# Performance work log

Hardware: AMD Instinct MI355X
Metric: run time of the kernel (lower is better)

## Reference

```python
import jax, jax.numpy as jnp
import numpy as np

# dims
IMG = 24; B = 2; C = 3; N = IMG * IMG + 1        # 577 tokens (patch size 1 + cls)
DIM = 512; DEPTH = 2; H = 8; DH = 64; MLP = 2048; NCLS = 1000
SW = 32      # sliding window size
CB = 16      # compress block size
CS = 4       # compress block sliding stride
SB = 64      # selection block size
KSEL = 4     # num selected blocks


def _ln(x, g, b):
    m = x.mean(-1, keepdims=True)
    v = ((x - m) ** 2).mean(-1, keepdims=True)
    return (x - m) * jax.lax.rsqrt(v + 1e-5) * g + b


# gather rows per (batch, head): t [n, d], i [n, m] -> [n, m, d]
_gather = jax.vmap(jax.vmap(lambda t, i: t[i]))


def _sparse_attn(x, Wq, Wk, Wv, Wg, Wo, kpe, vpe, Wkc, Wvc):
    """Native-sparse-attention (non-causal): compress + top-k block select + sliding window,
    combined with per-head sigmoid gates computed from the input."""
    b, n, _ = x.shape
    split = lambda t: t.reshape(b, n, H, DH).transpose(0, 2, 1, 3)   # [b,h,n,dh]
    q = split(x @ Wq); k = split(x @ Wk); v = split(x @ Wv)
    scale = DH ** -0.5

    # ---- compressed branch: overlapping blocks of size CB, stride CS, MLP-compressed ----
    nc = -(-n // CS)
    pad = (nc - 1) * CS + CB - n
    kp = jnp.pad(k, ((0, 0), (0, 0), (0, pad), (0, 0)))
    vp = jnp.pad(v, ((0, 0), (0, 0), (0, pad), (0, 0)))
    widx = jnp.arange(nc)[:, None] * CS + jnp.arange(CB)[None, :]    # [nc, CB]
    kw = kp[:, :, widx] + kpe                                        # [b,h,nc,CB,dh]
    vw = vp[:, :, widx] + vpe
    ck = kw.reshape(b, H, nc, CB * DH) @ Wkc                         # [b,h,nc,dh]
    cv = vw.reshape(b, H, nc, CB * DH) @ Wvc
    sc = jnp.einsum('bhid,bhjd->bhij', q, ck) * scale                # [b,h,n,nc]
    pc = jax.nn.softmax(sc, axis=-1)
    out_c = jnp.einsum('bhij,bhjd->bhid', pc, cv)

    # ---- selection branch: map compressed-block scores to selection blocks, top-k ----
    ns = -(-n // SB)
    centers = jnp.clip((jnp.arange(nc) * CS + CB // 2) // SB, 0, ns - 1)
    M = jax.nn.one_hot(centers, ns, dtype=pc.dtype)                  # [nc, ns]
    imp = jnp.einsum('bhij,js->bhis', pc, M)                         # [b,h,n,ns]
    _, selb = jax.lax.top_k(imp, KSEL)                               # [b,h,n,KSEL]
    tok = (selb[..., None] * SB + jnp.arange(SB)).reshape(b, H, n, KSEL * SB)
    mask = tok < n
    tokc = jnp.minimum(tok, n - 1)
    kg = _gather(k, tokc)                                            # [b,h,n,KSEL*SB,dh]
    vg = _gather(v, tokc)
    ss = jnp.einsum('bhid,bhikd->bhik', q, kg) * scale
    ss = jnp.where(mask, ss, -jnp.inf)
    ps = jax.nn.softmax(ss, axis=-1)
    out_s = jnp.einsum('bhik,bhikd->bhid', ps, vg)

    # ---- sliding window branch ----
    off = jnp.arange(SW) - SW // 2
    pos = jnp.arange(n)[:, None] + off                               # [n, SW]
    wmask = (pos >= 0) & (pos < n)
    posc = jnp.clip(pos, 0, n - 1)
    kwn = k[:, :, posc]; vwn = v[:, :, posc]                         # [b,h,n,SW,dh]
    sw = jnp.einsum('bhid,bhiwd->bhiw', q, kwn) * scale
    sw = jnp.where(wmask, sw, -jnp.inf)
    pw = jax.nn.softmax(sw, axis=-1)
    out_w = jnp.einsum('bhiw,bhiwd->bhid', pw, vwn)

    # ---- gated combine ----
    g = jax.nn.sigmoid(x @ Wg).reshape(b, n, H, 3).transpose(0, 2, 1, 3)  # [b,h,n,3]
    out = g[..., 0:1] * out_c + g[..., 1:2] * out_s + g[..., 2:3] * out_w
    return out.transpose(0, 2, 1, 3).reshape(b, n, H * DH) @ Wo


def _forward(img, patch_w, patch_b, pos_emb, cls_tok, ln1_g, ln1_b, Wq, Wk, Wv,
             Wg, Wo, kpe, vpe, Wkc, Wvc, ln2_g, ln2_b, ff_w1, ff_b1, ff_w2,
             ff_b2, hln_g, hln_b, head_w, head_b):
    b = img.shape[0]
    # patch size 1: b c h w -> b (h w) c, then linear embed
    x = img.transpose(0, 2, 3, 1).reshape(b, IMG * IMG, C) @ patch_w + patch_b
    x = jnp.concatenate([jnp.broadcast_to(cls_tok, (b, 1, DIM)), x], axis=1)
    x = x + pos_emb[:, :x.shape[1]]
    for l in range(DEPTH):
        h = _ln(x, ln1_g[l], ln1_b[l])
        x = _sparse_attn(h, Wq[l], Wk[l], Wv[l], Wg[l], Wo[l], kpe[l], vpe[l], Wkc[l], Wvc[l]) + x
        h = _ln(x, ln2_g[l], ln2_b[l])
        x = (jax.nn.gelu(h @ ff_w1[l] + ff_b1[l]) @ ff_w2[l] + ff_b2[l]) + x
    x = _ln(x[:, 0], hln_g, hln_b)   # cls pool + head LayerNorm
    return x @ head_w + head_b


def setup_inputs() -> dict:
    key = jax.random.key(0)
    ks = jax.random.split(key, 20)
    rn = lambda k, shape, s=0.02: jax.random.normal(k, shape, dtype=jnp.float32) * s
    d = {}
    d['img'] = jax.random.normal(ks[0], (B, C, IMG, IMG), dtype=jnp.float32)
    d['patch_w'] = rn(ks[1], (C, DIM), 0.2)
    d['patch_b'] = jnp.zeros((DIM,), jnp.float32)
    d['pos_emb'] = rn(ks[2], (1, N, DIM))
    d['cls_tok'] = rn(ks[3], (1, 1, DIM))
    d['ln1_g'] = jnp.ones((DEPTH, DIM), jnp.float32)
    d['ln1_b'] = jnp.zeros((DEPTH, DIM), jnp.float32)
    d['Wq'] = rn(ks[4], (DEPTH, DIM, H * DH))
    d['Wk'] = rn(ks[5], (DEPTH, DIM, H * DH))
    d['Wv'] = rn(ks[6], (DEPTH, DIM, H * DH))
    d['Wg'] = rn(ks[7], (DEPTH, DIM, 3 * H))
    d['Wo'] = rn(ks[8], (DEPTH, H * DH, DIM))
    d['kpe'] = rn(ks[9], (DEPTH, CB, DH))
    d['vpe'] = rn(ks[10], (DEPTH, CB, DH))
    d['Wkc'] = rn(ks[11], (DEPTH, CB * DH, DH))
    d['Wvc'] = rn(ks[12], (DEPTH, CB * DH, DH))
    d['ln2_g'] = jnp.ones((DEPTH, DIM), jnp.float32)
    d['ln2_b'] = jnp.zeros((DEPTH, DIM), jnp.float32)
    d['ff_w1'] = rn(ks[13], (DEPTH, DIM, MLP))
    d['ff_b1'] = jnp.zeros((DEPTH, MLP), jnp.float32)
    d['ff_w2'] = rn(ks[14], (DEPTH, MLP, DIM))
    d['ff_b2'] = jnp.zeros((DEPTH, DIM), jnp.float32)
    d['hln_g'] = jnp.ones((DIM,), jnp.float32)
    d['hln_b'] = jnp.zeros((DIM,), jnp.float32)
    d['head_w'] = rn(ks[15], (DIM, NCLS))
    d['head_b'] = jnp.zeros((NCLS,), jnp.float32)
    return d


def reference(img, patch_w, patch_b, pos_emb, cls_tok, ln1_g, ln1_b, Wq, Wk, Wv,
              Wg, Wo, kpe, vpe, Wkc, Wvc, ln2_g, ln2_b, ff_w1, ff_b1, ff_w2,
              ff_b2, hln_g, hln_b, head_w, head_b):
    return _forward(img, patch_w, patch_b, pos_emb, cls_tok, ln1_g, ln1_b, Wq, Wk, Wv,
                    Wg, Wo, kpe, vpe, Wkc, Wvc, ln2_g, ln2_b, ff_w1, ff_b1, ff_w2,
                    ff_b2, hln_g, hln_b, head_w, head_b)
```

## Files before the change

kernel.cpp:

```cpp
#include <hip/hip_runtime.h>
#include <math.h>


#define NTOK 577
#define DIMD 512
#define NH 8
#define DHD 64
#define NC 145
#define NSB 10
#define KSELD 4
#define SBD 64
#define CBD 16
#define CSD 4
#define SWD 32
#define MLPD 2048
#define NCLSD 1000
#define BATCH 2
#define QKVN 1536
#define QKVNG 1600
#define SFSTRIDE 592
#define SCSTRIDE 160
#define PSTRIDE 832
#define MCKD 2320

typedef unsigned short ushort;
typedef __attribute__((ext_vector_type(8))) short short8;
typedef __attribute__((ext_vector_type(4))) short short4v;
typedef __attribute__((ext_vector_type(4))) float f32x4;

__device__ __forceinline__ ushort bf16_rne(float f) {
  union { float f; unsigned u; } v; v.f = f;
  unsigned u = v.u;
  unsigned r = (u + 0x7fffu + ((u >> 16) & 1u)) >> 16;
  return (ushort)r;
}
__device__ __forceinline__ float bf16_to_f(ushort s) {
  union { unsigned u; float f; } v; v.u = ((unsigned)s) << 16;
  return v.f;
}
__device__ __forceinline__ int imin(int a, int b) { return a < b ? a : b; }
__device__ __forceinline__ int imax(int a, int b) { return a > b ? a : b; }

__global__ void patch_kernel(const float* __restrict__ img, const float* __restrict__ pw,
                             const float* __restrict__ pb, const float* __restrict__ pos,
                             const float* __restrict__ cls, float* __restrict__ x) {
  int idx = blockIdx.x * 256 + threadIdx.x;
  const int total = BATCH * NTOK * DIMD;
  if (idx >= total) return;
  int d = idx & (DIMD - 1);
  int i = (idx / DIMD) % NTOK;
  int b = idx / (DIMD * NTOK);
  float val;
  if (i == 0) {
    val = cls[d];
  } else {
    int p = i - 1;
    val = pb[d];
#pragma unroll
    for (int c = 0; c < 3; ++c)
      val += img[b * 3 * 576 + c * 576 + p] * pw[c * DIMD + d];
  }
  x[idx] = val + pos[i * DIMD + d];
}

__global__ void ln_kernel(const float* __restrict__ x, const float* __restrict__ g,
                          const float* __restrict__ bb, ushort* __restrict__ out_bf) {
  int row = blockIdx.x;
  const float* xr = x + (long)row * DIMD;
  int t = threadIdx.x;
  float a = xr[t], c = xr[t + 256];
  __shared__ float s1[256], s2[256];
  s1[t] = a + c;
  s2[t] = a * a + c * c;
  __syncthreads();
  for (int off = 128; off > 0; off >>= 1) {
    if (t < off) { s1[t] += s1[t + off]; s2[t] += s2[t + off]; }
    __syncthreads();
  }
  float m = s1[0] * (1.0f / 512.0f);
  float var = s2[0] * (1.0f / 512.0f) - m * m;
  float r = rsqrtf(var + 1e-5f);
  out_bf[(long)row * DIMD + t] = bf16_rne((a - m) * r * g[t] + bb[t]);
  out_bf[(long)row * DIMD + t + 256] = bf16_rne((c - m) * r * g[t + 256] + bb[t + 256]);
}

__global__ void wtrans_all_kernel(const float* __restrict__ Wq, const float* __restrict__ Wk,
                                  const float* __restrict__ Wv, const float* __restrict__ Wg,
                                  const float* __restrict__ Wo, const float* __restrict__ Wkc,
                                  const float* __restrict__ Wvc, const float* __restrict__ w1,
                                  const float* __restrict__ w2,
                                  ushort* __restrict__ wqkv_t, ushort* __restrict__ wo_t,
                                  ushort* __restrict__ w1_t, ushort* __restrict__ w2_t,
                                  ushort* __restrict__ wkc_t, ushort* __restrict__ wvc_t) {
  __shared__ float tile[32][33];
  int l = blockIdx.y;
  int t = blockIdx.x;
  const float* W; ushort* Wt; int K, N, bx, by;
  if (t < 768) {
    int which = t >> 8, rr = t & 255;
    W = (which == 0 ? Wq : (which == 1 ? Wk : Wv)) + (long)l * 512 * 512;
    Wt = wqkv_t + (long)l * QKVNG * 512 + which * 512 * 512;
    K = 512; N = 512; bx = rr & 15; by = rr >> 4;
  } else if (t < 1024) {
    int rr = t - 768; W = Wo + (long)l * 512 * 512; Wt = wo_t + (long)l * 512 * 512;
    K = 512; N = 512; bx = rr & 15; by = rr >> 4;
  } else if (t < 2048) {
    int rr = t - 1024; W = w1 + (long)l * 512 * 2048; Wt = w1_t + (long)l * 2048 * 512;
    K = 512; N = 2048; bx = rr & 63; by = rr >> 6;
  } else if (t < 3072) {
    int rr = t - 2048; W = w2 + (long)l * 2048 * 512; Wt = w2_t + (long)l * 512 * 2048;
    K = 2048; N = 512; bx = rr & 15; by = rr >> 4;
  } else if (t < 3104) {
    int rr = t - 3072; W = Wg + (long)l * 512 * 24;
    Wt = wqkv_t + (long)l * QKVNG * 512 + (long)1536 * 512;
    K = 512; N = 24; bx = rr & 1; by = rr >> 1;
  } else if (t < 3168) {
    int rr = t - 3104; W = Wkc + (long)l * 1024 * 64; Wt = wkc_t + (long)l * 64 * 1024;
    K = 1024; N = 64; bx = rr & 1; by = rr >> 1;
  } else {
    int rr = t - 3168; W = Wvc + (long)l * 1024 * 64; Wt = wvc_t + (long)l * 64 * 1024;
    K = 1024; N = 64; bx = rr & 1; by = rr >> 1;
  }
  int k0 = by * 32, n0 = bx * 32;
  int tx = threadIdx.x, ty = threadIdx.y;
#pragma unroll
  for (int r = 0; r < 32; r += 8)
    tile[ty + r][tx] = (n0 + tx < N) ? W[(long)(k0 + ty + r) * N + n0 + tx] : 0.f;
  __syncthreads();
#pragma unroll
  for (int r = 0; r < 32; r += 8)
    Wt[(long)(n0 + ty + r) * K + k0 + tx] = bf16_rne(tile[tx][ty + r]);
}

__global__ __launch_bounds__(256) void mfma_gemm(
    const ushort* __restrict__ A, const ushort* __restrict__ Bt,
    const float* __restrict__ bias,
    float* __restrict__ Cf, ushort* __restrict__ Cbf, float* __restrict__ gb,
    int M, int N, int K, int kSlice, int mode) {
  __shared__ short As[64][72];
  __shared__ short Bs[64][72];
  int tid = threadIdx.x;
  int lane = tid & 63, wave = tid >> 6;
  int wm = wave >> 1, wn = wave & 1;
  int rowBase = blockIdx.y * 64, colBase = blockIdx.x * 64;
  int m = lane & 15, kg = lane >> 4;
  int kBeg = blockIdx.z * kSlice;
  int kEnd = imin(K, kBeg + kSlice);
  f32x4 acc[2][2] = {};
  for (int k0 = kBeg; k0 < kEnd; k0 += 64) {
#pragma unroll
    for (int cc = 0; cc < 2; ++cc) {
      int c = tid * 2 + cc;
      int r = c >> 3, kc = c & 7;
      short8 av = {};
      int gr = rowBase + r;
      if (gr < M) av = *(const short8*)(A + (long)gr * K + k0 + kc * 8);
      *(short8*)&As[r][kc * 8] = av;
      short8 bv = *(const short8*)(Bt + (long)(colBase + r) * K + k0 + kc * 8);
      *(short8*)&Bs[r][kc * 8] = bv;
    }
    __syncthreads();
#pragma unroll
    for (int ks = 0; ks < 2; ++ks) {
      short8 a0 = *(const short8*)&As[wm * 32 + m][ks * 32 + kg * 8];
      short8 a1 = *(const short8*)&As[wm * 32 + 16 + m][ks * 32 + kg * 8];
      short8 b0 = *(const short8*)&Bs[wn * 32 + m][ks * 32 + kg * 8];
      short8 b1 = *(const short8*)&Bs[wn * 32 + 16 + m][ks * 32 + kg * 8];
      acc[0][0] = __builtin_amdgcn_mfma_f32_16x16x32_bf16(a0, b0, acc[0][0], 0, 0, 0);
      acc[0][1] = __builtin_amdgcn_mfma_f32_16x16x32_bf16(a0, b1, acc[0][1], 0, 0, 0);
      acc[1][0] = __builtin_amdgcn_mfma_f32_16x16x32_bf16(a1, b0, acc[1][0], 0, 0, 0);
      acc[1][1] = __builtin_amdgcn_mfma_f32_16x16x32_bf16(a1, b1, acc[1][1], 0, 0, 0);
    }
    __syncthreads();
  }
#pragma unroll
  for (int mt = 0; mt < 2; ++mt)
#pragma unroll
    for (int nt = 0; nt < 2; ++nt) {
      int col = colBase + wn * 32 + nt * 16 + m;
#pragma unroll
      for (int r = 0; r < 4; ++r) {
        int row = rowBase + wm * 32 + mt * 16 + kg * 4 + r;
        if (row >= M) continue;
        float v = acc[mt][nt][r];
        if (mode == 2) {
          if (col < QKVN) Cbf[(long)row * QKVN + col] = bf16_rne(v);
          else if (col < QKVNG) gb[(long)row * 64 + (col - QKVN)] = 1.f / (1.f + __expf(-v));
        } else if (mode == 1) {
          v += bias[col];
          float u = 0.7978845608028654f * (v + 0.044715f * v * v * v);
          v = 0.5f * v * (1.f + tanhf(u));
          Cbf[(long)row * N + col] = bf16_rne(v);
        } else {
          if (bias && blockIdx.z == 0) v += bias[col];
          atomicAdd(&Cf[(long)row * N + col], v);
        }
      }
    }
}

__global__ __launch_bounds__(256) void ckcv_gemm(
    const ushort* __restrict__ kwm, const ushort* __restrict__ vwm,
    const ushort* __restrict__ wkc_t, const ushort* __restrict__ wvc_t,
    ushort* __restrict__ ckb, ushort* __restrict__ Vt) {
  const int K = 1024;
  bool cvpath = blockIdx.z != 0;
  const ushort* A  = cvpath ? wvc_t : kwm;
  const ushort* Bt = cvpath ? vwm : wkc_t;
  int rowBase = cvpath ? 0 : blockIdx.y * 64;
  int colBase = cvpath ? blockIdx.y * 64 : 0;
  int aRows = cvpath ? 64 : MCKD;
  int bRows = cvpath ? MCKD : 64;
  __shared__ short As[64][72];
  __shared__ short Bs[64][72];
  int tid = threadIdx.x;
  int lane = tid & 63, wave = tid >> 6;
  int wm = wave >> 1, wn = wave & 1;
  int m = lane & 15, kg = lane >> 4;
  f32x4 acc[2][2] = {};
  for (int k0 = 0; k0 < K; k0 += 64) {
#pragma unroll
    for (int cc = 0; cc < 2; ++cc) {
      int c = tid * 2 + cc;
      int r = c >> 3, kc = c & 7;
      short8 av = {};
      if (rowBase + r < aRows) av = *(const short8*)(A + (long)(rowBase + r) * K + k0 + kc * 8);
      *(short8*)&As[r][kc * 8] = av;
      short8 bv = {};
      if (colBase + r < bRows) bv = *(const short8*)(Bt + (long)(colBase + r) * K + k0 + kc * 8);
      *(short8*)&Bs[r][kc * 8] = bv;
    }
    __syncthreads();
#pragma unroll
    for (int ks = 0; ks < 2; ++ks) {
      short8 a0 = *(const short8*)&As[wm * 32 + m][ks * 32 + kg * 8];
      short8 a1 = *(const short8*)&As[wm * 32 + 16 + m][ks * 32 + kg * 8];
      short8 b0 = *(const short8*)&Bs[wn * 32 + m][ks * 32 + kg * 8];
      short8 b1 = *(const short8*)&Bs[wn * 32 + 16 + m][ks * 32 + kg * 8];
      acc[0][0] = __builtin_amdgcn_mfma_f32_16x16x32_bf16(a0, b0, acc[0][0], 0, 0, 0);
      acc[0][1] = __builtin_amdgcn_mfma_f32_16x16x32_bf16(a0, b1, acc[0][1], 0, 0, 0);
      acc[1][0] = __builtin_amdgcn_mfma_f32_16x16x32_bf16(a1, b0, acc[1][0], 0, 0, 0);
      acc[1][1] = __builtin_amdgcn_mfma_f32_16x16x32_bf16(a1, b1, acc[1][1], 0, 0, 0);
    }
    __syncthreads();
  }
#pragma unroll
  for (int mt = 0; mt < 2; ++mt)
#pragma unroll
    for (int nt = 0; nt < 2; ++nt) {
      int col = colBase + wn * 32 + nt * 16 + m;
#pragma unroll
      for (int r = 0; r < 4; ++r) {
        int row = rowBase + wm * 32 + mt * 16 + kg * 4 + r;
        float v = acc[mt][nt][r];
        if (!cvpath) {
          if (row < MCKD) ckb[(long)row * DHD + col] = bf16_rne(v);
        } else {
          if (col < MCKD) {
            int z16 = col / NC, j = col - z16 * NC;
            Vt[((long)z16 * 64 + row) * PSTRIDE + 640 + j] = bf16_rne(v);
          }
        }
      }
    }
}

__global__ __launch_bounds__(256) void score_kernel(
    const ushort* __restrict__ qkv_bf, const ushort* __restrict__ ckb,
    ushort* __restrict__ Sf, ushort* __restrict__ Scb, float scale) {
  __shared__ short As[64][72];
  __shared__ short Bs[64][72];
  int z = blockIdx.z;
  int b = z >> 3, h = z & 7;
  int i0 = blockIdx.y * 64;
  int xb = blockIdx.x;
  bool isC = xb >= 10;
  int j0 = (isC ? (xb - 10) : xb) * 64;
  int tid = threadIdx.x;
  int lane = tid & 63, wave = tid >> 6;
  int wm = wave >> 1, wn = wave & 1;
  const ushort* aBase = qkv_bf + (long)b * NTOK * QKVN + h * 64;
  const ushort* bBase = aBase + 512;
  const ushort* cBase = ckb + (long)z * NC * DHD;
#pragma unroll
  for (int rep = 0; rep < 4; ++rep) {
    int row = rep * 16 + (tid >> 4);
    int c4 = tid & 15;
    int gi = i0 + row;
    short4v a16 = {};
    if (gi < NTOK) a16 = *(const short4v*)(aBase + (long)gi * QKVN + c4 * 4);
    *(short4v*)&As[row][c4 * 4] = a16;
    int gj = j0 + row;
    short4v b16 = {};
    if (isC) {
      if (gj < NC) b16 = *(const short4v*)(cBase + (long)gj * DHD + c4 * 4);
    } else {
      if (gj < NTOK) b16 = *(const short4v*)(bBase + (long)gj * QKVN + c4 * 4);
    }
    *(short4v*)&Bs[row][c4 * 4] = b16;
  }
  __syncthreads();
  int m = lane & 15, kg = lane >> 4;
  f32x4 acc[2][2] = {};
#pragma unroll
  for (int ks = 0; ks < 2; ++ks) {
    short8 a0 = *(const short8*)&As[wm * 32 + m][ks * 32 + kg * 8];
    short8 a1 = *(const short8*)&As[wm * 32 + 16 + m][ks * 32 + kg * 8];
    short8 b0 = *(const short8*)&Bs[wn * 32 + m][ks * 32 + kg * 8];
    short8 b1 = *(const short8*)&Bs[wn * 32 + 16 + m][ks * 32 + kg * 8];
    acc[0][0] = __builtin_amdgcn_mfma_f32_16x16x32_bf16(a0, b0, acc[0][0], 0, 0, 0);
    acc[0][1] = __builtin_amdgcn_mfma_f32_16x16x32_bf16(a0, b1, acc[0][1], 0, 0, 0);
    acc[1][0] = __builtin_amdgcn_mfma_f32_16x16x32_bf16(a1, b0, acc[1][0], 0, 0, 0);
    acc[1][1] = __builtin_amdgcn_mfma_f32_16x16x32_bf16(a1, b1, acc[1][1], 0, 0, 0);
  }
  int nvalid = isC ? NC : NTOK;
  int sstride = isC ? SCSTRIDE : SFSTRIDE;
  ushort* Sz = (isC ? Scb : Sf) + (long)z * NTOK * sstride;
#pragma unroll
  for (int mt = 0; mt < 2; ++mt)
#pragma unroll
    for (int nt = 0; nt < 2; ++nt) {
      int col = j0 + wn * 32 + nt * 16 + m;
#pragma unroll
      for (int r = 0; r < 4; ++r) {
        int row = i0 + wm * 32 + mt * 16 + kg * 4 + r;
        if (row < NTOK && col < nvalid)
          Sz[(long)row * sstride + col] = bf16_rne(acc[mt][nt][r] * scale);
      }
    }
}

__global__ void kwvt_kernel(const ushort* __restrict__ qkv_bf,
                            const float* __restrict__ kpe, const float* __restrict__ vpe,
                            ushort* __restrict__ kwm, ushort* __restrict__ vwm,
                            ushort* __restrict__ Vt) {
  __shared__ short tile[64][72];
  int bid = blockIdx.x;
  if (bid < MCKD) {
    int j = bid % NC;
    int bh = bid / NC;
    int h = bh & 7, b = bh >> 3;
    int t = threadIdx.x >> 4;
    int d4 = threadIdx.x & 15;
    int tok = j * CSD + t;
    float k0 = 0.f, k1 = 0.f, k2 = 0.f, k3 = 0.f, v0 = 0.f, v1 = 0.f, v2 = 0.f, v3 = 0.f;
    if (tok < NTOK) {
      const ushort* base = qkv_bf + (long)(b * NTOK + tok) * QKVN + h * DHD + d4 * 4;
      short4v kv = *(const short4v*)(base + 512);
      short4v vv = *(const short4v*)(base + 1024);
      k0 = bf16_to_f((ushort)kv.x); k1 = bf16_to_f((ushort)kv.y);
      k2 = bf16_to_f((ushort)kv.z); k3 = bf16_to_f((ushort)kv.w);
      v0 = bf16_to_f((ushort)vv.x); v1 = bf16_to_f((ushort)vv.y);
      v2 = bf16_to_f((ushort)vv.z); v3 = bf16_to_f((ushort)vv.w);
    }
    float4 kp = *(const float4*)(kpe + t * DHD + d4 * 4);
    float4 vp = *(const float4*)(vpe + t * DHD + d4 * 4);
    short4v ko, vo;
    ko.x = (short)bf16_rne(k0 + kp.x); ko.y = (short)bf16_rne(k1 + kp.y);
    ko.z = (short)bf16_rne(k2 + kp.z); ko.w = (short)bf16_rne(k3 + kp.w);
    vo.x = (short)bf16_rne(v0 + vp.x); vo.y = (short)bf16_rne(v1 + vp.y);
    vo.z = (short)bf16_rne(v2 + vp.z); vo.w = (short)bf16_rne(v3 + vp.w);
    long ob = (long)bid * 1024 + t * DHD + d4 * 4;
    *(short4v*)(kwm + ob) = ko;
    *(short4v*)(vwm + ob) = vo;
  } else {
    int t = bid - MCKD;
    int kt = t % 10, z = t / 10;
    int b = z >> 3, h = z & 7;
    int tid = threadIdx.x;
    int r = tid >> 2, seg = tid & 3;
    short8 a0 = {}, a1 = {};
    int tok = kt * 64 + r;
    if (tok < NTOK) {
      const ushort* src = qkv_bf + (long)(b * NTOK + tok) * QKVN + 1024 + h * 64 + seg * 16;
      a0 = *(const short8*)src;
      a1 = *(const short8*)(src + 8);
    }
    *(short8*)&tile[r][seg * 16] = a0;
    *(short8*)&tile[r][seg * 16 + 8] = a1;
    __syncthreads();
    int d = tid >> 2;
    short8 o0, o1;
#pragma unroll
    for (int q = 0; q < 8; ++q) o0[q] = tile[seg * 16 + q][d];
#pragma unroll
    for (int q = 0; q < 8; ++q) o1[q] = tile[seg * 16 + 8 + q][d];
    ushort* dst = Vt + ((long)z * 64 + d) * PSTRIDE + kt * 64 + seg * 16;
    *(short8*)dst = o0;
    *(short8*)(dst + 8) = o1;
  }
}

__global__ __launch_bounds__(256, 4) void prob_kernel(
    const ushort* __restrict__ Sf, const ushort* __restrict__ Scb,
    const float* __restrict__ gb, ushort* __restrict__ P) {
  int qt = blockIdx.x % NC;
  int z = blockIdx.x / NC;
  int h = z & 7, b = z >> 3;
  int tid = threadIdx.x, lane = tid & 63, w = tid >> 6;
  int i0 = qt * 4 + w;
  bool valid = i0 < NTOK;
  int i = imin(i0, NTOK - 1);

  __shared__ float scL[4][192];
  __shared__ float ssL[4][256];
  __shared__ float swL[4][32];
  __shared__ float impL[4][16];
  __shared__ int selL[4][KSELD];
  float* sc = scL[w]; float* ss = ssL[w];
  float* swv = swL[w]; float* imp = impL[w]; int* sel = selL[w];

  const ushort* scRow = Scb + ((long)z * NTOK + i) * SCSTRIDE;
  const ushort* sfRow = Sf + ((long)z * NTOK + i) * SFSTRIDE;

  float e[3], mC = -1e30f;
#pragma unroll
  for (int c = 0; c < 3; ++c) {
    int j = c * 64 + lane;
    float s = bf16_to_f(scRow[imin(j, NC - 1)]);
    s = (j < NC) ? s : -1e30f;
    e[c] = s;
    mC = fmaxf(mC, s);
  }
#pragma unroll
  for (int msk = 1; msk < 64; msk <<= 1) mC = fmaxf(mC, __shfl_xor(mC, msk, 64));
  float sumC = 0.f;
#pragma unroll
  for (int c = 0; c < 3; ++c) {
    float ev = (e[c] > -1e29f) ? __expf(e[c] - mC) : 0.f;
    sc[c * 64 + lane] = ev;
    sumC += ev;
  }
#pragma unroll
  for (int msk = 1; msk < 64; msk <<= 1) sumC += __shfl_xor(sumC, msk, 64);
  __syncthreads();

  if (lane < NSB) {
    int lo = imax(0, 16 * lane - 2), hi = imin(NC - 1, 16 * lane + 13);
    float s = 0.f;
    for (int j = lo; j <= hi; ++j) s += sc[j];
    imp[lane] = s;
  }
  __syncthreads();
  if (lane == 0) {
    unsigned used = 0;
    for (int r = 0; r < KSELD; ++r) {
      int bi = 0; float bv = -1e30f;
      for (int s = 0; s < NSB; ++s)
        if (!((used >> s) & 1u) && imp[s] > bv) { bv = imp[s]; bi = s; }
      used |= 1u << bi;
      sel[r] = bi;
    }
  }
  __syncthreads();

  float es[4], mS = -1e30f;
#pragma unroll
  for (int c = 0; c < 4; ++c) {
    int tok = sel[c] * SBD + lane;
    float s = bf16_to_f(sfRow[imin(tok, NTOK - 1)]);
    s = (tok < NTOK) ? s : -1e30f;
    es[c] = s;
    mS = fmaxf(mS, s);
  }
#pragma unroll
  for (int msk = 1; msk < 64; msk <<= 1) mS = fmaxf(mS, __shfl_xor(mS, msk, 64));
  float sumS = 0.f;
#pragma unroll
  for (int c = 0; c < 4; ++c) {
    float ev = (es[c] > -1e29f) ? __expf(es[c] - mS) : 0.f;
    ss[c * 64 + lane] = ev;
    sumS += ev;
  }
#pragma unroll
  for (int msk = 1; msk < 64; msk <<= 1) sumS += __shfl_xor(sumS, msk, 64);

  float sw_s;
  {
    int pos = i + (lane & 31) - SWD / 2;
    float s = bf16_to_f(sfRow[imin(imax(pos, 0), NTOK - 1)]);
    sw_s = (pos >= 0 && pos < NTOK) ? s : -1e30f;
  }
  float mW = sw_s;
#pragma unroll
  for (int msk = 1; msk < 32; msk <<= 1) mW = fmaxf(mW, __shfl_xor(mW, msk, 64));
  float ew = (sw_s > -1e29f) ? __expf(sw_s - mW) : 0.f;
  float sumW = ew;
#pragma unroll
  for (int msk = 1; msk < 32; msk <<= 1) sumW += __shfl_xor(sumW, msk, 64);
  if (lane < SWD) swv[lane] = ew;
  __syncthreads();

  if (!valid) return;
  const float* gp = gb + (long)(b * NTOK + i) * 64 + h * 3;
  float rC = gp[0] / sumC, rS = gp[1] / sumS, rW = gp[2] / sumW;
  ushort* prow = P + ((long)z * NTOK + i0) * PSTRIDE;
#pragma unroll
  for (int c = 0; c < 10; ++c) {
    int col = c * 64 + lane;
    float val = 0.f;
#pragma unroll
    for (int r = 0; r < 4; ++r)
      if (sel[r] == c) val += rS * ss[r * 64 + lane];
    int t = col - i + 16;
    if (t >= 0 && t < SWD && col < NTOK) val += rW * swv[t];
    prow[col] = bf16_rne(val);
  }
#pragma unroll
  for (int c = 0; c < 3; ++c) {
    int j = c * 64 + lane;
    float val = (j < NC) ? rC * sc[j] : 0.f;
    prow[640 + j] = bf16_rne(val);
  }
}

__global__ __launch_bounds__(256) void pv_gemm(const ushort* __restrict__ P,
                                               const ushort* __restrict__ Vt,
                                               ushort* __restrict__ comb) {
  __shared__ short As[64][72];
  __shared__ short Bs[64][72];
  int z = blockIdx.y;
  int b = z >> 3, h = z & 7;
  int rowBase = blockIdx.x * 64;
  int tid = threadIdx.x;
  int lane = tid & 63, wave = tid >> 6;
  int wm = wave >> 1, wn = wave & 1;
  const ushort* Pz = P + (long)z * NTOK * PSTRIDE;
  const ushort* Vz = Vt + (long)z * 64 * PSTRIDE;
  int m = lane & 15, kg = lane >> 4;
  f32x4 acc[2][2] = {};
  for (int k0 = 0; k0 < PSTRIDE; k0 += 64) {
#pragma unroll
    for (int cc = 0; cc < 2; ++cc) {
      int c = tid * 2 + cc;
      int r = c >> 3, kc = c & 7;
      short8 av = {};
      int gr = rowBase + r;
      if (gr < NTOK) av = *(const short8*)(Pz + (long)gr * PSTRIDE + k0 + kc * 8);
      *(short8*)&As[r][kc * 8] = av;
      short8 bv = *(const short8*)(Vz + (long)r * PSTRIDE + k0 + kc * 8);
      *(short8*)&Bs[r][kc * 8] = bv;
    }
    __syncthreads();
#pragma unroll
    for (int ks = 0; ks < 2; ++ks) {
      short8 a0 = *(const short8*)&As[wm * 32 + m][ks * 32 + kg * 8];
      short8 a1 = *(const short8*)&As[wm * 32 + 16 + m][ks * 32 + kg * 8];
      short8 b0 = *(const short8*)&Bs[wn * 32 + m][ks * 32 + kg * 8];
      short8 b1 = *(const short8*)&Bs[wn * 32 + 16 + m][ks * 32 + kg * 8];
      acc[0][0] = __builtin_amdgcn_mfma_f32_16x16x32_bf16(a0, b0, acc[0][0], 0, 0, 0);
      acc[0][1] = __builtin_amdgcn_mfma_f32_16x16x32_bf16(a0, b1, acc[0][1], 0, 0, 0);
      acc[1][0] = __builtin_amdgcn_mfma_f32_16x16x32_bf16(a1, b0, acc[1][0], 0, 0, 0);
      acc[1][1] = __builtin_amdgcn_mfma_f32_16x16x32_bf16(a1, b1, acc[1][1], 0, 0, 0);
    }
    __syncthreads();
  }
#pragma unroll
  for (int mt = 0; mt < 2; ++mt)
#pragma unroll
    for (int nt = 0; nt < 2; ++nt) {
      int col = wn * 32 + nt * 16 + m;
#pragma unroll
      for (int r = 0; r < 4; ++r) {
        int row = rowBase + wm * 32 + mt * 16 + kg * 4 + r;
        if (row < NTOK)
          comb[(long)(b * NTOK + row) * DIMD + h * 64 + col] = bf16_rne(acc[mt][nt][r]);
      }
    }
}

__global__ void head_kernel(const float* __restrict__ x, const float* __restrict__ hg,
                            const float* __restrict__ hb, const float* __restrict__ W,
                            const float* __restrict__ bias, float* __restrict__ out) {
  int b = blockIdx.y;
  int tid = threadIdx.x;
  const float* xr = x + (long)b * NTOK * DIMD;
  __shared__ float red1[256], red2[256];
  float a = xr[tid], c = xr[tid + 256];
  red1[tid] = a + c;
  red2[tid] = a * a + c * c;
  __syncthreads();
  for (int off = 128; off > 0; off >>= 1) {
    if (tid < off) { red1[tid] += red1[tid + off]; red2[tid] += red2[tid + off]; }
    __syncthreads();
  }
  float m = red1[0] * (1.f / 512.f);
  float var = red2[0] * (1.f / 512.f) - m * m;
  float rs = rsqrtf(var + 1e-5f);
  __shared__ float hs[512];
  hs[tid] = (a - m) * rs * hg[tid] + hb[tid];
  hs[tid + 256] = (c - m) * rs * hg[tid + 256] + hb[tid + 256];
  __syncthreads();
  int col = blockIdx.x * 64 + (tid & 63);
  int ks = tid >> 6;
  float acc = 0.f;
  if (col < NCLSD) {
    for (int k = ks * 128; k < ks * 128 + 128; ++k)
      acc += hs[k] * W[(long)k * NCLSD + col];
  }
  __shared__ float part[4][64];
  part[ks][tid & 63] = acc;
  __syncthreads();
  if (tid < 64) {
    int c2 = blockIdx.x * 64 + tid;
    if (c2 < NCLSD)
      out[b * NCLSD + c2] = part[0][tid] + part[1][tid] + part[2][tid] + part[3][tid] + bias[c2];
  }
}

extern "C" void kernel_launch(void* const* d_in, const int* in_sizes, int n_in,
                              void* d_out, int out_size, void* d_ws, size_t ws_size,
                              hipStream_t stream) {
  const float* img     = (const float*)d_in[0];
  const float* patch_w = (const float*)d_in[1];
  const float* patch_b = (const float*)d_in[2];
  const float* pos_emb = (const float*)d_in[3];
  const float* cls_tok = (const float*)d_in[4];
  const float* ln1_g   = (const float*)d_in[5];
  const float* ln1_b   = (const float*)d_in[6];
  const float* Wq      = (const float*)d_in[7];
  const float* Wk      = (const float*)d_in[8];
  const float* Wv      = (const float*)d_in[9];
  const float* Wg      = (const float*)d_in[10];
  const float* Wo      = (const float*)d_in[11];
  const float* kpe     = (const float*)d_in[12];
  const float* vpe     = (const float*)d_in[13];
  const float* Wkc     = (const float*)d_in[14];
  const float* Wvc     = (const float*)d_in[15];
  const float* ln2_g   = (const float*)d_in[16];
  const float* ln2_b   = (const float*)d_in[17];
  const float* ff_w1   = (const float*)d_in[18];
  const float* ff_b1   = (const float*)d_in[19];
  const float* ff_w2   = (const float*)d_in[20];
  const float* ff_b2   = (const float*)d_in[21];
  const float* hln_g   = (const float*)d_in[22];
  const float* hln_b   = (const float*)d_in[23];
  const float* head_w  = (const float*)d_in[24];
  const float* head_b  = (const float*)d_in[25];
  float* out = (float*)d_out;

  char* p = (char*)d_ws;
  const long MROW = (long)BATCH * NTOK;
  float* x       = (float*)p;  p += MROW * DIMD * 4;
  ushort* qkv_bf = (ushort*)p; p += MROW * QKVN * 2;
  ushort* h_bf   = (ushort*)p; p += MROW * DIMD * 2;
  ushort* comb_bf= (ushort*)p; p += MROW * DIMD * 2;
  float* gb      = (float*)p;  p += MROW * 64 * 4;
  ushort* ckb    = (ushort*)p; p += (long)MCKD * DHD * 2;
  ushort* Vt     = (ushort*)p; p += (long)BATCH * NH * 64 * PSTRIDE * 2;
  ushort* Scb    = (ushort*)p; p += (long)BATCH * NH * NTOK * SCSTRIDE * 2;
  ushort* wqkv_t = (ushort*)p; p += 2L * QKVNG * DIMD * 2;
  ushort* wo_t   = (ushort*)p; p += 2L * DIMD * DIMD * 2;
  ushort* w1_t   = (ushort*)p; p += 2L * MLPD * DIMD * 2;
  ushort* w2_t   = (ushort*)p; p += 2L * DIMD * MLPD * 2;
  ushort* wkc_t  = (ushort*)p; p += 2L * 64 * 1024 * 2;
  ushort* wvc_t  = (ushort*)p; p += 2L * 64 * 1024 * 2;
  ushort* kwm    = (ushort*)p;
  ushort* vwm    = kwm + (long)MCKD * 1024;
  ushort* P      = kwm;
  p += (long)BATCH * NH * NTOK * PSTRIDE * 2;
  ushort* Sf     = (ushort*)p;
  ushort* ff1_bf = Sf;
  p += (long)BATCH * NH * NTOK * SFSTRIDE * 2;

  const int M = (int)MROW;
  const int MB64 = (M + 63) / 64;
  const float scale = 0.125f;
  dim3 thrT(32, 8);

  patch_kernel<<<(M * DIMD + 255) / 256, 256, 0, stream>>>(img, patch_w, patch_b, pos_emb, cls_tok, x);
  wtrans_all_kernel<<<dim3(3232, 2), thrT, 0, stream>>>(Wq, Wk, Wv, Wg, Wo, Wkc, Wvc,
                                                        ff_w1, ff_w2, wqkv_t, wo_t, w1_t, w2_t,
                                                        wkc_t, wvc_t);

  for (int l = 0; l < 2; ++l) {
    const ushort* wqkv_l = wqkv_t + (long)l * QKVNG * DIMD;
    const ushort* wo_l   = wo_t + (long)l * DIMD * DIMD;
    const ushort* w1t_l  = w1_t + (long)l * MLPD * DIMD;
    const ushort* w2t_l  = w2_t + (long)l * DIMD * MLPD;
    const ushort* wkc_l  = wkc_t + (long)l * 64 * 1024;
    const ushort* wvc_l  = wvc_t + (long)l * 64 * 1024;
    const float* kpe_l = kpe + (long)l * CBD * DHD;
    const float* vpe_l = vpe + (long)l * CBD * DHD;
    const float* b1_l  = ff_b1 + (long)l * MLPD;
    const float* b2_l  = ff_b2 + (long)l * DIMD;

    ln_kernel<<<M, 256, 0, stream>>>(x, ln1_g + (long)l * DIMD, ln1_b + (long)l * DIMD, h_bf);
    mfma_gemm<<<dim3(QKVNG / 64, MB64), 256, 0, stream>>>(h_bf, wqkv_l, nullptr, nullptr, qkv_bf, gb, M, QKVNG, DIMD, DIMD, 2);
    kwvt_kernel<<<MCKD + 160, 256, 0, stream>>>(qkv_bf, kpe_l, vpe_l, kwm, vwm, Vt);
    ckcv_gemm<<<dim3(1, (MCKD + 63) / 64, 2), 256, 0, stream>>>(kwm, vwm, wkc_l, wvc_l, ckb, Vt);
    score_kernel<<<dim3(13, 10, BATCH * NH), 256, 0, stream>>>(qkv_bf, ckb, Sf, Scb, scale);
    prob_kernel<<<BATCH * NH * NC, 256, 0, stream>>>(Sf, Scb, gb, P);
    pv_gemm<<<dim3(10, BATCH * NH), 256, 0, stream>>>(P, Vt, comb_bf);
    mfma_gemm<<<dim3(DIMD / 64, MB64, 2), 256, 0, stream>>>(comb_bf, wo_l, nullptr, x, nullptr, nullptr, M, DIMD, DIMD, 256, 4);
    ln_kernel<<<M, 256, 0, stream>>>(x, ln2_g + (long)l * DIMD, ln2_b + (long)l * DIMD, h_bf);
    mfma_gemm<<<dim3(MLPD / 64, MB64), 256, 0, stream>>>(h_bf, w1t_l, b1_l, nullptr, ff1_bf, nullptr, M, MLPD, DIMD, DIMD, 1);
    mfma_gemm<<<dim3(DIMD / 64, MB64, 4), 256, 0, stream>>>(ff1_bf, w2t_l, b2_l, x, nullptr, nullptr, M, DIMD, MLPD, 512, 4);
  }

  head_kernel<<<dim3(16, BATCH), 256, 0, stream>>>(x, hln_g, hln_b, head_w, head_b, out);
}
```

Measured before the change: 379.4 us.

## Use direct global-to-LDS loads with XOR swizzle in GEMM and fuse prep kernels

```diff
diff --git a/kernel.cpp b/kernel.cpp
--- a/kernel.cpp
+++ b/kernel.cpp
@@ -28,6 +28,20 @@
 typedef __attribute__((ext_vector_type(4))) short short4v;
 typedef __attribute__((ext_vector_type(4))) float f32x4;
 
+#if defined(__has_builtin)
+#if __has_builtin(__builtin_amdgcn_global_load_lds)
+#define HAVE_GLL 1
+#endif
+#endif
+
+#ifdef HAVE_GLL
+__device__ __forceinline__ void gll16(const ushort* g, short* l) {
+  __builtin_amdgcn_global_load_lds(
+      (const __attribute__((address_space(1))) unsigned int*)g,
+      (__attribute__((address_space(3))) unsigned int*)l, 16, 0, 0);
+}
+#endif
+
 __device__ __forceinline__ ushort bf16_rne(float f) {
   union { float f; unsigned u; } v; v.f = f;
   unsigned u = v.u;
@@ -41,60 +55,42 @@
 __device__ __forceinline__ int imin(int a, int b) { return a < b ? a : b; }
 __device__ __forceinline__ int imax(int a, int b) { return a > b ? a : b; }
 
-__global__ void patch_kernel(const float* __restrict__ img, const float* __restrict__ pw,
-                             const float* __restrict__ pb, const float* __restrict__ pos,
-                             const float* __restrict__ cls, float* __restrict__ x) {
-  int idx = blockIdx.x * 256 + threadIdx.x;
-  const int total = BATCH * NTOK * DIMD;
-  if (idx >= total) return;
-  int d = idx & (DIMD - 1);
-  int i = (idx / DIMD) % NTOK;
-  int b = idx / (DIMD * NTOK);
-  float val;
-  if (i == 0) {
-    val = cls[d];
-  } else {
-    int p = i - 1;
-    val = pb[d];
-#pragma unroll
-    for (int c = 0; c < 3; ++c)
-      val += img[b * 3 * 576 + c * 576 + p] * pw[c * DIMD + d];
-  }
-  x[idx] = val + pos[i * DIMD + d];
-}
-
-__global__ void ln_kernel(const float* __restrict__ x, const float* __restrict__ g,
-                          const float* __restrict__ bb, ushort* __restrict__ out_bf) {
-  int row = blockIdx.x;
-  const float* xr = x + (long)row * DIMD;
-  int t = threadIdx.x;
-  float a = xr[t], c = xr[t + 256];
-  __shared__ float s1[256], s2[256];
-  s1[t] = a + c;
-  s2[t] = a * a + c * c;
-  __syncthreads();
-  for (int off = 128; off > 0; off >>= 1) {
-    if (t < off) { s1[t] += s1[t + off]; s2[t] += s2[t + off]; }
-    __syncthreads();
-  }
-  float m = s1[0] * (1.0f / 512.0f);
-  float var = s2[0] * (1.0f / 512.0f) - m * m;
-  float r = rsqrtf(var + 1e-5f);
-  out_bf[(long)row * DIMD + t] = bf16_rne((a - m) * r * g[t] + bb[t]);
-  out_bf[(long)row * DIMD + t + 256] = bf16_rne((c - m) * r * g[t + 256] + bb[t + 256]);
-}
-
-__global__ void wtrans_all_kernel(const float* __restrict__ Wq, const float* __restrict__ Wk,
-                                  const float* __restrict__ Wv, const float* __restrict__ Wg,
-                                  const float* __restrict__ Wo, const float* __restrict__ Wkc,
-                                  const float* __restrict__ Wvc, const float* __restrict__ w1,
-                                  const float* __restrict__ w2,
-                                  ushort* __restrict__ wqkv_t, ushort* __restrict__ wo_t,
-                                  ushort* __restrict__ w1_t, ushort* __restrict__ w2_t,
-                                  ushort* __restrict__ wkc_t, ushort* __restrict__ wvc_t) {
+__global__ void prep_kernel(const float* __restrict__ Wq, const float* __restrict__ Wk,
+                            const float* __restrict__ Wv, const float* __restrict__ Wg,
+                            const float* __restrict__ Wo, const float* __restrict__ Wkc,
+                            const float* __restrict__ Wvc, const float* __restrict__ w1,
+                            const float* __restrict__ w2,
+                            ushort* __restrict__ wqkv_t, ushort* __restrict__ wo_t,
+                            ushort* __restrict__ w1_t, ushort* __restrict__ w2_t,
+                            ushort* __restrict__ wkc_t, ushort* __restrict__ wvc_t,
+                            const float* __restrict__ img, const float* __restrict__ pw,
+                            const float* __restrict__ pb, const float* __restrict__ pos,
+                            const float* __restrict__ cls, float* __restrict__ x) {
+  int bid = blockIdx.x;
+  int tid = threadIdx.x;
+  if (bid >= 6464) {
+    int idx = (bid - 6464) * 256 + tid;
+    const int total = BATCH * NTOK * DIMD;
+    if (idx >= total) return;
+    int d = idx & (DIMD - 1);
+    int i = (idx / DIMD) % NTOK;
+    int b = idx / (DIMD * NTOK);
+    float val;
+    if (i == 0) {
+      val = cls[d];
+    } else {
+      int p = i - 1;
+      val = pb[d];
+#pragma unroll
+      for (int c = 0; c < 3; ++c)
+        val += img[b * 3 * 576 + c * 576 + p] * pw[c * DIMD + d];
+    }
+    x[idx] = val + pos[i * DIMD + d];
+    return;
+  }
   __shared__ float tile[32][33];
-  int l = blockIdx.y;
-  int t = blockIdx.x;
+  int l = bid / 3232;
+  int t = bid % 3232;
   const float* W; ushort* Wt; int K, N, bx, by;
   if (t < 768) {
     int which = t >> 8, rr = t & 255;
@@ -122,7 +118,7 @@
     K = 1024; N = 64; bx = rr & 1; by = rr >> 1;
   }
   int k0 = by * 32, n0 = bx * 32;
-  int tx = threadIdx.x, ty = threadIdx.y;
+  int tx = tid & 31, ty = tid >> 5;
 #pragma unroll
   for (int r = 0; r < 32; r += 8)
     tile[ty + r][tx] = (n0 + tx < N) ? W[(long)(k0 + ty + r) * N + n0 + tx] : 0.f;
@@ -130,6 +126,27 @@
 #pragma unroll
   for (int r = 0; r < 32; r += 8)
     Wt[(long)(n0 + ty + r) * K + k0 + tx] = bf16_rne(tile[tx][ty + r]);
+}
+
+__global__ void ln_kernel(const float* __restrict__ x, const float* __restrict__ g,
+                          const float* __restrict__ bb, ushort* __restrict__ out_bf) {
+  int row = blockIdx.x;
+  const float* xr = x + (long)row * DIMD;
+  int t = threadIdx.x;
+  float a = xr[t], c = xr[t + 256];
+  __shared__ float s1[256], s2[256];
+  s1[t] = a + c;
+  s2[t] = a * a + c * c;
+  __syncthreads();
+  for (int off = 128; off > 0; off >>= 1) {
+    if (t < off) { s1[t] += s1[t + off]; s2[t] += s2[t + off]; }
+    __syncthreads();
+  }
+  float m = s1[0] * (1.0f / 512.0f);
+  float var = s2[0] * (1.0f / 512.0f) - m * m;
+  float r = rsqrtf(var + 1e-5f);
+  out_bf[(long)row * DIMD + t] = bf16_rne((a - m) * r * g[t] + bb[t]);
+  out_bf[(long)row * DIMD + t + 256] = bf16_rne((c - m) * r * g[t + 256] + bb[t + 256]);
 }
 
 __global__ __launch_bounds__(256) void mfma_gemm(
@@ -137,8 +154,6 @@
     const float* __restrict__ bias,
     float* __restrict__ Cf, ushort* __restrict__ Cbf, float* __restrict__ gb,
     int M, int N, int K, int kSlice, int mode) {
-  __shared__ short As[64][72];
-  __shared__ short Bs[64][72];
   int tid = threadIdx.x;
   int lane = tid & 63, wave = tid >> 6;
   int wm = wave >> 1, wn = wave & 1;
@@ -147,6 +162,43 @@
   int kBeg = blockIdx.z * kSlice;
   int kEnd = imin(K, kBeg + kSlice);
   f32x4 acc[2][2] = {};
+#ifdef HAVE_GLL
+  __shared__ short As[64 * 64];
+  __shared__ short Bs[64 * 64];
+  int r8 = lane >> 3;
+  int cs = (lane & 7) ^ r8;
+  const ushort* aG0 = A + (long)(rowBase + wave * 8 + r8) * K + cs * 8 + kBeg;
+  const ushort* aG1 = aG0 + (long)32 * K;
+  const ushort* bG0 = Bt + (long)(colBase + wave * 8 + r8) * K + cs * 8 + kBeg;
+  const ushort* bG1 = bG0 + (long)32 * K;
+  short* lA0 = &As[(wave * 8) * 64];
+  short* lA1 = &As[(wave * 8 + 32) * 64];
+  short* lB0 = &Bs[(wave * 8) * 64];
+  short* lB1 = &Bs[(wave * 8 + 32) * 64];
+  int xa = m & 7;
+  for (int k0 = 0; k0 < kEnd - kBeg; k0 += 64) {
+    gll16(aG0 + k0, lA0);
+    gll16(aG1 + k0, lA1);
+    gll16(bG0 + k0, lB0);
+    gll16(bG1 + k0, lB1);
+    __syncthreads();
+#pragma unroll
+    for (int ks = 0; ks < 2; ++ks) {
+      int kc = ks * 4 + kg;
+      short8 a0 = *(const short8*)&As[(wm * 32 + m) * 64 + (kc ^ xa) * 8];
+      short8 a1 = *(const short8*)&As[(wm * 32 + 16 + m) * 64 + (kc ^ xa) * 8];
+      short8 b0 = *(const short8*)&Bs[(wn * 32 + m) * 64 + (kc ^ xa) * 8];
+      short8 b1 = *(const short8*)&Bs[(wn * 32 + 16 + m) * 64 + (kc ^ xa) * 8];
+      acc[0][0] = __builtin_amdgcn_mfma_f32_16x16x32_bf16(a0, b0, acc[0][0], 0, 0, 0);
+      acc[0][1] = __builtin_amdgcn_mfma_f32_16x16x32_bf16(a0, b1, acc[0][1], 0, 0, 0);
+      acc[1][0] = __builtin_amdgcn_mfma_f32_16x16x32_bf16(a1, b0, acc[1][0], 0, 0, 0);
+      acc[1][1] = __builtin_amdgcn_mfma_f32_16x16x32_bf16(a1, b1, acc[1][1], 0, 0, 0);
+    }
+    __syncthreads();
+  }
+#else
+  __shared__ short As[64][72];
+  __shared__ short Bs[64][72];
   for (int k0 = kBeg; k0 < kEnd; k0 += 64) {
 #pragma unroll
     for (int cc = 0; cc < 2; ++cc) {
@@ -173,6 +225,7 @@
     }
     __syncthreads();
   }
+#endif
 #pragma unroll
   for (int mt = 0; mt < 2; ++mt)
 #pragma unroll
@@ -662,16 +715,16 @@
   ushort* Sf     = (ushort*)p;
   ushort* ff1_bf = Sf;
   p += (long)BATCH * NH * NTOK * SFSTRIDE * 2;
+  p += 64 * 2048 * 2;
 
   const int M = (int)MROW;
   const int MB64 = (M + 63) / 64;
   const float scale = 0.125f;
-  dim3 thrT(32, 8);
-
-  patch_kernel<<<(M * DIMD + 255) / 256, 256, 0, stream>>>(img, patch_w, patch_b, pos_emb, cls_tok, x);
-  wtrans_all_kernel<<<dim3(3232, 2), thrT, 0, stream>>>(Wq, Wk, Wv, Wg, Wo, Wkc, Wvc,
-                                                        ff_w1, ff_w2, wqkv_t, wo_t, w1_t, w2_t,
-                                                        wkc_t, wvc_t);
+
+  prep_kernel<<<6464 + (int)((M * DIMD + 255) / 256), 256, 0, stream>>>(
+      Wq, Wk, Wv, Wg, Wo, Wkc, Wvc, ff_w1, ff_w2,
+      wqkv_t, wo_t, w1_t, w2_t, wkc_t, wvc_t,
+      img, patch_w, patch_b, pos_emb, cls_tok, x);
 
   for (int l = 0; l < 2; ++l) {
     const ushort* wqkv_l = wqkv_t + (long)l * QKVNG * DIMD;
```

New measurement: 364.7 us. -3.9%, faster.
